# Kernel tuning notes

Measured on AMD Instinct MI355X. Metric: run time of the kernel, lower is better.

Reference implementation:

```python
import jax, jax.numpy as jnp
import numpy as np

B = 32; N = 512; SEQ_LEN = 8
L = 0.05; T_REF = 5.0; V_TH = 20.0; V_RES = 0.0
SQL = float(np.sqrt(L))
BN_EPS = 1e-5

# ---- Dawson-style lookup tables for the LIF moment activation (built once, float64) ----
_XG = np.linspace(-10.0, 4.0, 7001)
_DX = _XG[1] - _XG[0]

def _cumtrapz(y):
    return np.concatenate([[0.0], np.cumsum(0.5 * (y[1:] + y[:-1]) * _DX)])

_phi = np.exp(-_XG ** 2)
_I = np.exp(-100.0) / 20.0 + _cumtrapz(_phi)          # int_{-inf}^x e^{-t^2} dt (asymptotic tail at -10)
_g = np.exp(_XG ** 2) * _I                             # 1st Dawson-like function g(x)
_G = _cumtrapz(_g)                                     # int g dx (rel. to -10)
_h = np.exp(_XG ** 2) * _cumtrapz(_phi * _g ** 2)      # 2nd Dawson-like function h(x)
_H = _cumtrapz(_h)                                     # int h dx

XG = jnp.asarray(_XG, jnp.float32)
GT = jnp.asarray(_g, jnp.float32)
GI = jnp.asarray(_G, jnp.float32)
HI = jnp.asarray(_H, jnp.float32)

def _interp(x, tab):
    return jnp.interp(x, XG, tab)

def moment_activate(u, s, rho):
    # Mnn_Activate_Mean / Std / Corr: LIF moment activation
    s = jnp.maximum(s, 1e-6)
    ub = jnp.clip((V_TH * L - u) / (s * SQL), -10.0, 4.0)
    lb = jnp.clip((V_RES * L - u) / (s * SQL), -10.0, 4.0)
    dG = _interp(ub, GI) - _interp(lb, GI)
    ua = 1.0 / (T_REF + (2.0 / L) * dG)                               # mean firing rate
    dH = jnp.maximum(_interp(ub, HI) - _interp(lb, HI), 0.0)
    sa = jnp.sqrt((8.0 / L ** 2) * dH * ua ** 3)                      # firing std
    dg = _interp(ub, GT) - _interp(lb, GT)
    chi = ua ** 2 * (2.0 / L) * dg / (SQL * jnp.maximum(sa, 1e-9))    # linear response coeff
    eye = jnp.eye(rho.shape[-1], dtype=rho.dtype)
    rho_out = chi[:, :, None] * chi[:, None, :] * rho                 # [B,N,N]
    rho_out = rho_out * (1.0 - eye) + eye                             # unit diagonal
    return ua, sa, rho_out

def linear_corr(W, b, u, s, rho):
    # Mnn_Linear_Corr: mean via affine map, covariance via W C W^T
    u_out = u @ W.T + b
    Cin = rho * s[:, :, None] * s[:, None, :]                         # [B,N,N] covariance
    C = jnp.einsum('bik,lk->bil', jnp.einsum('ij,bjk->bik', W, Cin), W)
    var = jnp.clip(jnp.diagonal(C, axis1=1, axis2=2), 0.0, None)
    s_out = jnp.sqrt(var)
    denom = s_out[:, :, None] * s_out[:, None, :]
    rho_out = jnp.where(denom > 1e-12, C / jnp.maximum(denom, 1e-12), 0.0)
    return u_out, s_out, rho_out

def mexi_hat(n, k=0.3):
    dx = 2.0 * np.pi / n
    x = np.arange(0.0, 2.0 * np.pi, dx)[:n]
    y = np.exp(2.0 * (np.cos(x) - 1.0)) * np.cos(2.0 * x)
    j = np.arange(n)
    idx = (j[None, :] - j[:, None]) % n                               # w[i,:] = y.roll(i)
    return y[idx].astype(np.float32)

def setup_inputs() -> dict:
    ks = jax.random.split(jax.random.key(0), 10)
    u = jax.random.normal(ks[0], (B, N), jnp.float32)
    s = jax.random.uniform(ks[1], (B, N), jnp.float32, 0.1, 1.0)
    A = jax.random.normal(ks[2], (B, N, N), jnp.float32) / np.sqrt(N)
    sym = 0.5 * (A + jnp.swapaxes(A, 1, 2))
    eye = jnp.eye(N, dtype=jnp.float32)
    rho = jnp.clip(sym, -0.5, 0.5) * (1.0 - eye) + eye                # valid-ish corr matrix
    u_ext = jax.random.normal(ks[3], (B, N), jnp.float32)
    s_ext = jax.random.uniform(ks[4], (B, N), jnp.float32, 0.1, 1.0)
    W = 0.02 * jax.random.normal(ks[5], (N, N), jnp.float32) + 0.1 * jnp.asarray(mexi_hat(N))
    b = 0.02 * jax.random.normal(ks[6], (N,), jnp.float32)
    W_ext = 0.02 * jax.random.normal(ks[7], (N, N), jnp.float32)
    b_ext = 0.02 * jax.random.normal(ks[8], (N,), jnp.float32)
    w_mean = 2.5 * jnp.ones((N,), jnp.float32)
    b_mean = 2.5 * jnp.ones((N,), jnp.float32)
    w_mean_ext = 2.5 * jnp.ones((N,), jnp.float32)
    b_mean_ext = 2.5 * jnp.ones((N,), jnp.float32)
    return {'u': u, 's': s, 'rho': rho, 'u_ext': u_ext, 's_ext': s_ext,
            'W': W, 'b': b, 'W_ext': W_ext, 'b_ext': b_ext,
            'w_mean': w_mean, 'b_mean': b_mean,
            'w_mean_ext': w_mean_ext, 'b_mean_ext': b_mean_ext,
            'seq_len': SEQ_LEN}

def reference(u, s, rho, u_ext, s_ext, W, b, W_ext, b_ext,
              w_mean, b_mean, w_mean_ext, b_mean_ext, seq_len):
    # external pathway (Mnn_Linear_without_Corr + BN), computed once
    u_e = u_ext @ W_ext.T + b_ext
    s_e = jnp.sqrt((s_ext ** 2) @ (W_ext ** 2).T)
    mean_e = jnp.mean(u_e, axis=0); var_e = jnp.var(u_e, axis=0)
    f_e = w_mean_ext / jnp.sqrt(var_e + BN_EPS)
    s_e = s_e * jnp.abs(f_e)                                          # Mnn_Std_Bn1d (uses pre-BN stats)
    u_e = (u_e - mean_e) * f_e + b_mean_ext

    def step(carry, _):
        u, s, rho = carry
        u, s, rho = linear_corr(W, b, u, s, rho)
        mean = jnp.mean(u, axis=0); var = jnp.var(u, axis=0)
        f = w_mean / jnp.sqrt(var + BN_EPS)
        s = s * jnp.abs(f)
        u = (u - mean) * f + b_mean
        u = u + u_e
        s = jnp.sqrt(s * s + s_e * s_e)
        return moment_activate(u, s, rho), None

    (u, s, rho), _ = jax.lax.scan(step, (u, s, rho), None, length=seq_len)
    return u, s, rho
```

## Files before the change

### kernel.cpp

```cpp
#include <hip/hip_runtime.h>
#include <math.h>


#define BB 32
#define NN 512
#define SEQ 8
#define TG 7001
#define SVN (BB * NN)

typedef float f32x4 __attribute__((ext_vector_type(4)));
typedef short s16x8 __attribute__((ext_vector_type(8)));

__device__ __forceinline__ unsigned short bf16_rne(float v) {
    unsigned u = __float_as_uint(v);
    u += 0x7FFFu + ((u >> 16) & 1u);
    return (unsigned short)(u >> 16);
}
__device__ __forceinline__ float bf16_f(unsigned short h) {
    return __uint_as_float(((unsigned)h) << 16);
}
__device__ __forceinline__ void split2(float v, unsigned short& h, unsigned short& l) {
    unsigned short hh = bf16_rne(v);
    h = hh;
    l = bf16_rne(v - bf16_f(hh));
}

__device__ __forceinline__ size_t ts_idx(int r, int k) {
    return (size_t)(((r >> 4) * 16 + (k >> 5)) * 512 + ((k >> 3) & 3) * 128 + (r & 15) * 8 + (k & 7));
}

__device__ __forceinline__ float interp_tab(const float* __restrict__ tab, float x) {
    float t = (x + 10.0f) * 500.0f;
    t = fminf(fmaxf(t, 0.0f), 7000.0f);
    int i0 = (int)t;
    if (i0 > 6999) i0 = 6999;
    float fr = t - (float)i0;
    float a = tab[i0];
    float b = tab[i0 + 1];
    return fmaf(fr, b - a, a);
}

__global__ void k_exp(double* __restrict__ expP, double* __restrict__ expM) {
    int k = blockIdx.x * 256 + threadIdx.x;
    if (k >= TG) return;
    double x = -10.0 + (14.0 / 7000.0) * k;
    expP[k] = exp(x * x);
    expM[k] = exp(-x * x);
}

__device__ double blk_exscan(double part, double* wsum) {
    int t = threadIdx.x, lane = t & 63, wid = t >> 6;
    double run = part;
    #pragma unroll
    for (int off = 1; off < 64; off <<= 1) {
        double nv = __shfl_up(run, off);
        if (lane >= off) run += nv;
    }
    if (lane == 63) wsum[wid] = run;
    __syncthreads();
    if (t < 16) {
        double v = wsum[t];
        #pragma unroll
        for (int off = 1; off < 16; off <<= 1) {
            double nv = __shfl_up(v, off);
            if (lane >= off) v += nv;
        }
        wsum[t] = v;
    }
    __syncthreads();
    double base = (wid > 0) ? wsum[wid - 1] : 0.0;
    double ex = base + run - part;
    __syncthreads();
    return ex;
}

__global__ __launch_bounds__(1024)
void k_scan(const double* __restrict__ expP, const double* __restrict__ expM,
            float* __restrict__ GT, float* __restrict__ GI, float* __restrict__ HI) {
    __shared__ double ys[7008];
    __shared__ double wsum[16];
    const int t = threadIdx.x;
    const double dx = 14.0 / 7000.0;
    int k0 = t * 7, k1 = k0 + 7;
    if (k1 > TG) k1 = TG;
    if (k0 > TG) k0 = TG;
    int kls = (k0 < 1) ? 1 : k0;

    for (int k = k0; k < k1; ++k) ys[k] = expM[k];
    __syncthreads();

    double tmp[7];
    {
        double part = 0.0;
        for (int k = kls; k < k1; ++k) part += 0.5 * (ys[k - 1] + ys[k]) * dx;
        double run = blk_exscan(part, wsum) + exp(-100.0) / 20.0;
        int c = 0;
        for (int k = k0; k < k1; ++k) {
            if (k >= 1) run += 0.5 * (ys[k - 1] + ys[k]) * dx;
            tmp[c] = expP[k] * run;
            GT[k] = (float)tmp[c];
            ++c;
        }
        __syncthreads();
        c = 0;
        for (int k = k0; k < k1; ++k) ys[k] = tmp[c++];
        __syncthreads();
    }
    {
        double part = 0.0;
        for (int k = kls; k < k1; ++k) part += 0.5 * (ys[k - 1] + ys[k]) * dx;
        double run = blk_exscan(part, wsum);
        for (int k = k0; k < k1; ++k) {
            if (k >= 1) run += 0.5 * (ys[k - 1] + ys[k]) * dx;
            GI[k] = (float)run;
        }
        __syncthreads();
    }
    {
        double part = 0.0;
        for (int k = kls; k < k1; ++k) {
            double ya = expM[k - 1] * ys[k - 1] * ys[k - 1];
            double yb = expM[k] * ys[k] * ys[k];
            part += 0.5 * (ya + yb) * dx;
        }
        double run = blk_exscan(part, wsum);
        int c = 0;
        for (int k = k0; k < k1; ++k) {
            if (k >= 1) {
                double ya = expM[k - 1] * ys[k - 1] * ys[k - 1];
                double yb = expM[k] * ys[k] * ys[k];
                run += 0.5 * (ya + yb) * dx;
            }
            tmp[c++] = run;
        }
        __syncthreads();
        c = 0;
        for (int k = k0; k < k1; ++k) ys[k] = tmp[c++];
        __syncthreads();
    }
    {
        double part = 0.0;
        for (int k = kls; k < k1; ++k)
            part += 0.5 * (expP[k - 1] * ys[k - 1] + expP[k] * ys[k]) * dx;
        double run = blk_exscan(part, wsum);
        for (int k = k0; k < k1; ++k) {
            if (k >= 1) run += 0.5 * (expP[k - 1] * ys[k - 1] + expP[k] * ys[k]) * dx;
            HI[k] = (float)run;
        }
    }
}

__global__ void k_splitW(const float* __restrict__ W,
                         unsigned short* __restrict__ Wh, unsigned short* __restrict__ Wl) {
    int t = blockIdx.x * 256 + threadIdx.x;
    int r = t >> 6, c8 = t & 63;
    int k = c8 * 8;
    const float* src = W + (size_t)r * NN + k;
    s16x8 hv, lv;
    #pragma unroll
    for (int q = 0; q < 8; ++q) {
        unsigned short h, l;
        split2(src[q], h, l);
        hv[q] = (short)h; lv[q] = (short)l;
    }
    size_t o = ts_idx(r, k);
    *reinterpret_cast<s16x8*>(Wh + o) = hv;
    *reinterpret_cast<s16x8*>(Wl + o) = lv;
}

__global__ void k_splitQ(const float* __restrict__ rho, const float* __restrict__ s,
                         unsigned short* __restrict__ Qh, unsigned short* __restrict__ Ql) {
    int t = blockIdx.x * 256 + threadIdx.x;
    int b = t >> 15;
    int rem = t & 32767;
    int r = rem >> 6, c8 = rem & 63;
    int k = c8 * 8;
    const float* src = rho + ((size_t)b * NN + r) * NN + k;
    const float* sb = s + b * NN;
    float si = sb[r];
    s16x8 hv, lv;
    #pragma unroll
    for (int q = 0; q < 8; ++q) {
        float v = src[q] * si * sb[k + q];
        unsigned short h, l;
        split2(v, h, l);
        hv[q] = (short)h; lv[q] = (short)l;
    }
    size_t o = (size_t)b * NN * NN + ts_idx(r, k);
    *reinterpret_cast<s16x8*>(Qh + o) = hv;
    *reinterpret_cast<s16x8*>(Ql + o) = lv;
}

#define LOADF(AH, AL, BH, BL, OFF)                                             \
    {                                                                          \
        _Pragma("unroll") for (int t_ = 0; t_ < 4; ++t_)                       \
            AH[t_] = *reinterpret_cast<const s16x8*>(pAh + t_ * 8192 + (OFF)); \
        _Pragma("unroll") for (int t_ = 0; t_ < 2; ++t_)                       \
            BH[t_] = *reinterpret_cast<const s16x8*>(pBh + t_ * 8192 + (OFF)); \
        _Pragma("unroll") for (int t_ = 0; t_ < 4; ++t_)                       \
            AL[t_] = *reinterpret_cast<const s16x8*>(pAl + t_ * 8192 + (OFF)); \
        _Pragma("unroll") for (int t_ = 0; t_ < 2; ++t_)                       \
            BL[t_] = *reinterpret_cast<const s16x8*>(pBl + t_ * 8192 + (OFF)); \
    }

#define MFMAF(AH, AL, BH, BL)                                                  \
    {                                                                          \
        _Pragma("unroll") for (int m_ = 0; m_ < 4; ++m_)                       \
            _Pragma("unroll") for (int n_ = 0; n_ < 2; ++n_)                   \
                acc[m_][n_] = __builtin_amdgcn_mfma_f32_16x16x32_bf16(         \
                    AH[m_], BH[n_], acc[m_][n_], 0, 0, 0);                     \
        _Pragma("unroll") for (int m_ = 0; m_ < 4; ++m_)                       \
            _Pragma("unroll") for (int n_ = 0; n_ < 2; ++n_)                   \
                acc[m_][n_] = __builtin_amdgcn_mfma_f32_16x16x32_bf16(         \
                    AL[m_], BH[n_], acc[m_][n_], 0, 0, 0);                     \
        _Pragma("unroll") for (int m_ = 0; m_ < 4; ++m_)                       \
            _Pragma("unroll") for (int n_ = 0; n_ < 2; ++n_)                   \
                acc[m_][n_] = __builtin_amdgcn_mfma_f32_16x16x32_bf16(         \
                    AH[m_], BL[n_], acc[m_][n_], 0, 0, 0);                     \
    }

template <int PHASE>
__global__ __launch_bounds__(512, 4)
void gemm_ts(const unsigned short* __restrict__ Ah, const unsigned short* __restrict__ Al,
             long aStride,
             const unsigned short* __restrict__ Bh, const unsigned short* __restrict__ Bl,
             long bStride,
             unsigned short* __restrict__ Oh, unsigned short* __restrict__ Ol,
             float* __restrict__ Of,
             const float* __restrict__ Wf, float* __restrict__ sv,
             const float* __restrict__ u_prev, const float* __restrict__ bvec,
             float* __restrict__ u_linT,
             const float* __restrict__ bn_w, const float* __restrict__ bmv,
             const float* __restrict__ u_e, const float* __restrict__ s_e2,
             const float* __restrict__ GT, const float* __restrict__ GI,
             const float* __restrict__ HI,
             float* __restrict__ u_next, float* __restrict__ s_next) {
    __shared__ __align__(16) unsigned short stg[8 * 4096];
    __shared__ float slS[256], chS[256], snS[256];

    const int id = blockIdx.x;
    const int member = (id >> 3) & 3;
    const int g = (id & 7) | ((id >> 5) << 3);
    const int p = g & 3;
    const int b = g >> 2;
    const int xt = (PHASE == 0) ? p : member;
    const int yt = (PHASE == 0) ? member : p;
    const int i0 = yt * 128, j0 = xt * 128;
    const int tid = threadIdx.x;
    const int w = tid >> 6, lane = tid & 63;
    const int wqm = w >> 2, wqn = w & 3;

    const int laneo = lane * 8;
    const unsigned short* pAh = Ah + (size_t)b * aStride + (size_t)((i0 >> 4) + wqm * 4) * 8192 + laneo;
    const unsigned short* pAl = Al + (size_t)b * aStride + (size_t)((i0 >> 4) + wqm * 4) * 8192 + laneo;
    const unsigned short* pBh = Bh + (size_t)b * bStride + (size_t)((j0 >> 4) + wqn * 2) * 8192 + laneo;
    const unsigned short* pBl = Bl + (size_t)b * bStride + (size_t)((j0 >> 4) + wqn * 2) * 8192 + laneo;

    if (PHASE == 0) {
        const int tile16 = yt * 4 + xt;
        const int row = tile16 * 32 + (tid >> 4);
        const int seg = tid & 15;
        const float4* wr = (const float4*)(Wf + (size_t)row * NN + seg * 32);
        const float4* ur = (const float4*)(u_prev + b * NN + seg * 32);
        float a0 = 0.f, a1 = 0.f, a2 = 0.f, a3 = 0.f;
        #pragma unroll
        for (int kk = 0; kk < 8; ++kk) {
            float4 wv = wr[kk], uv = ur[kk];
            a0 = fmaf(wv.x, uv.x, a0);
            a1 = fmaf(wv.y, uv.y, a1);
            a2 = fmaf(wv.z, uv.z, a2);
            a3 = fmaf(wv.w, uv.w, a3);
        }
        float au = (a0 + a1) + (a2 + a3);
        au += __shfl_xor(au, 1);
        au += __shfl_xor(au, 2);
        au += __shfl_xor(au, 4);
        au += __shfl_xor(au, 8);
        if (seg == 0) u_linT[row * BB + b] = au + bvec[row];
    } else if (tid < 256) {
        const int ii = (tid < 128) ? (i0 + tid) : (j0 + tid - 128);
        float vb[32];
        {
            const float4* ul = (const float4*)(u_linT + (size_t)ii * BB);
            #pragma unroll
            for (int q = 0; q < 8; ++q) {
                float4 t4 = ul[q];
                vb[q * 4 + 0] = t4.x; vb[q * 4 + 1] = t4.y;
                vb[q * 4 + 2] = t4.z; vb[q * 4 + 3] = t4.w;
            }
        }
        float m = 0.0f;
        #pragma unroll
        for (int bb = 0; bb < BB; ++bb) m += vb[bb];
        m *= (1.0f / BB);
        float v = 0.0f;
        #pragma unroll
        for (int bb = 0; bb < BB; ++bb) {
            float d = vb[bb] - m;
            v = fmaf(d, d, v);
        }
        v *= (1.0f / BB);
        float f = bn_w[ii] / sqrtf(v + 1e-5f);
        const int idx = b * NN + ii;
        float s2;
        {
            const float* svp = sv + idx;
            float q0 = (svp[0 * SVN] + svp[1 * SVN]) + (svp[2 * SVN] + svp[3 * SVN]);
            float q1 = (svp[4 * SVN] + svp[5 * SVN]) + (svp[6 * SVN] + svp[7 * SVN]);
            float q2 = (svp[8 * SVN] + svp[9 * SVN]) + (svp[10 * SVN] + svp[11 * SVN]);
            float q3 = (svp[12 * SVN] + svp[13 * SVN]) + (svp[14 * SVN] + svp[15 * SVN]);
            s2 = (q0 + q1) + (q2 + q3);
        }
        float s_l = sqrtf(fmaxf(s2, 0.0f));
        float un = fmaf(vb[b] - m, f, bmv[ii]) + u_e[idx];
        float sn = sqrtf(fmaf((s_l * s_l) * f, f, s_e2[idx]));
        const float SQL = 0.22360679774997896f;
        float ss = fmaxf(sn, 1e-6f);
        float inv = 1.0f / (ss * SQL);
        float ubx = fminf(fmaxf((1.0f - un) * inv, -10.0f), 4.0f);
        float lbx = fminf(fmaxf((0.0f - un) * inv, -10.0f), 4.0f);
        float dG = interp_tab(GI, ubx) - interp_tab(GI, lbx);
        float ua = 1.0f / fmaf(40.0f, dG, 5.0f);
        float dH = fmaxf(interp_tab(HI, ubx) - interp_tab(HI, lbx), 0.0f);
        float sa = sqrtf(3200.0f * dH * ua * ua * ua);
        float dg2 = interp_tab(GT, ubx) - interp_tab(GT, lbx);
        float ch = ua * ua * 40.0f * dg2 / (SQL * fmaxf(sa, 1e-9f));
        slS[tid] = s_l;
        chS[tid] = ch;
        snS[tid] = sa;
        if (i0 == j0 && tid < 128) {
            u_next[idx] = ua;
            s_next[idx] = sa;
        }
    }

    f32x4 acc[4][2];
    #pragma unroll
    for (int m2 = 0; m2 < 4; ++m2)
        #pragma unroll
        for (int n2 = 0; n2 < 2; ++n2) acc[m2][n2] = (f32x4){0.f, 0.f, 0.f, 0.f};

    s16x8 fah[4], fal[4], fbh[2], fbl[2];
    #pragma unroll 2
    for (int kb = 0; kb < 16; ++kb) {
        LOADF(fah, fal, fbh, fbl, kb * 512);
        MFMAF(fah, fal, fbh, fbl);
    }

    if (PHASE != 0) __syncthreads();

    const size_t bofs = (size_t)b * NN * NN;
    const int rb0 = i0 + wqm * 64 + (lane >> 4) * 4;
    const int cb0 = j0 + wqn * 32 + (lane & 15);

    if (PHASE == 0) {
        float dp[16];
        #pragma unroll
        for (int m2 = 0; m2 < 4; ++m2)
            #pragma unroll
            for (int r = 0; r < 4; ++r) {
                int row = rb0 + m2 * 16 + r;
                const float* wrow = Wf + ((size_t)row << 9) + cb0;
                float s = 0.0f;
                #pragma unroll
                for (int n2 = 0; n2 < 2; ++n2) s = fmaf(acc[m2][n2][r], wrow[n2 * 16], s);
                dp[m2 * 4 + r] = s;
            }
        #pragma unroll
        for (int k = 0; k < 16; ++k) {
            #pragma unroll
            for (int off = 1; off < 16; off <<= 1) dp[k] += __shfl_xor(dp[k], off);
        }
        if ((lane & 15) == 0) {
            float* svslot = sv + (size_t)(xt * 4 + wqn) * SVN + b * NN;
            #pragma unroll
            for (int k = 0; k < 16; ++k) {
                int row = rb0 + (k >> 2) * 16 + (k & 3);
                svslot[row] = dp[k];
            }
        }
    }

    if (PHASE == 2) {
        float* fS = (float*)stg + w * 2048;
        #pragma unroll
        for (int m2 = 0; m2 < 4; ++m2)
            #pragma unroll
            for (int r = 0; r < 4; ++r) {
                const int lr = m2 * 16 + (lane >> 4) * 4 + r;
                const float si = slS[wqm * 64 + lr], ci = chS[wqm * 64 + lr];
                const int row = i0 + wqm * 64 + lr;
                #pragma unroll
                for (int n2 = 0; n2 < 2; ++n2) {
                    const int lc = wqn * 32 + n2 * 16 + (lane & 15);
                    const float sj = slS[128 + lc], cj = chS[128 + lc];
                    const int col = j0 + lc;
                    float denom = si * sj;
                    float rv = (denom > 1e-12f) ? (acc[m2][n2][r] / fmaxf(denom, 1e-12f)) : 0.0f;
                    rv *= ci * cj;
                    if (row == col) rv = 1.0f;
                    fS[lr * 32 + n2 * 16 + (lane & 15)] = rv;
                }
            }
        #pragma unroll
        for (int inst = 0; inst < 8; ++inst) {
            const int row = i0 + wqm * 64 + inst * 8 + (lane >> 3);
            const int col = j0 + wqn * 32 + (lane & 7) * 4;
            *reinterpret_cast<f32x4*>(Of + bofs + ((size_t)row << 9) + col) =
                *reinterpret_cast<const f32x4*>(fS + inst * 256 + (lane >> 3) * 32 + (lane & 7) * 4);
        }
    } else {
        unsigned short* hiS = stg + w * 4096;
        unsigned short* loS = hiS + 2048;
        const int laneconst = (((lane & 15) >> 3) << 7) + ((lane >> 4) << 5) + (lane & 7);
        #pragma unroll
        for (int m2 = 0; m2 < 4; ++m2)
            #pragma unroll
            for (int n2 = 0; n2 < 2; ++n2) {
                const int base = laneconst + m2 * 512 + n2 * 256;
                #pragma unroll
                for (int r = 0; r < 4; ++r) {
                    float v;
                    if (PHASE == 0) {
                        v = acc[m2][n2][r];
                    } else {
                        const int lr = wqm * 64 + m2 * 16 + (lane >> 4) * 4 + r;
                        const int lc = wqn * 32 + n2 * 16 + (lane & 15);
                        const float si = slS[lr], ci = chS[lr], qi = snS[lr];
                        const float sj = slS[128 + lc], cj = chS[128 + lc], qj = snS[128 + lc];
                        float denom = si * sj;
                        float rv = (denom > 1e-12f) ? (acc[m2][n2][r] / fmaxf(denom, 1e-12f)) : 0.0f;
                        rv *= ci * cj;
                        if (i0 + lr == j0 + lc) rv = 1.0f;
                        v = rv * qi * qj;
                    }
                    unsigned short h, l;
                    split2(v, h, l);
                    hiS[base + r * 8] = h;
                    loS[base + r * 8] = l;
                }
            }
        #pragma unroll
        for (int lb = 0; lb < 4; ++lb) {
            const int gb = ((i0 >> 4) + wqm * 4 + lb) * 16 + (j0 >> 5) + wqn;
            *reinterpret_cast<s16x8*>(Oh + bofs + (size_t)gb * 512 + laneo) =
                *reinterpret_cast<const s16x8*>(hiS + lb * 512 + laneo);
            *reinterpret_cast<s16x8*>(Ol + bofs + (size_t)gb * 512 + laneo) =
                *reinterpret_cast<const s16x8*>(loS + lb * 512 + laneo);
        }
    }
}

__global__ void k_ext_dots(const float* __restrict__ Wx, const float* __restrict__ bx,
                           const float* __restrict__ ux, const float* __restrict__ sx,
                           float* __restrict__ u_e, float* __restrict__ s_e2) {
    int gw = (blockIdx.x << 2) + (threadIdx.x >> 6);
    int lane = threadIdx.x & 63;
    int b = gw >> 9, i = gw & 511;
    const float* wr = Wx + (size_t)i * NN;
    const float* ub = ux + b * NN;
    const float* sb = sx + b * NN;
    float au = 0.0f, as2 = 0.0f;
    for (int j = lane; j < NN; j += 64) {
        float w = wr[j];
        float s = sb[j];
        au = fmaf(w, ub[j], au);
        as2 = fmaf(w * w, s * s, as2);
    }
    #pragma unroll
    for (int off = 32; off; off >>= 1) {
        au += __shfl_down(au, off);
        as2 += __shfl_down(as2, off);
    }
    if (lane == 0) {
        u_e[b * NN + i] = au + bx[i];
        s_e2[b * NN + i] = as2;
    }
}

__global__ void k_ext_stats(float* __restrict__ u_e, float* __restrict__ s_e2,
                            const float* __restrict__ wmx, const float* __restrict__ bmx) {
    int i = blockIdx.x * blockDim.x + threadIdx.x;
    if (i >= NN) return;
    float m = 0.0f;
    for (int b = 0; b < BB; ++b) m += u_e[b * NN + i];
    m *= (1.0f / BB);
    float v = 0.0f;
    for (int b = 0; b < BB; ++b) {
        float d = u_e[b * NN + i] - m;
        v = fmaf(d, d, v);
    }
    v *= (1.0f / BB);
    float f = wmx[i] / sqrtf(v + 1e-5f);
    float bm = bmx[i];
    for (int b = 0; b < BB; ++b) {
        u_e[b * NN + i] = fmaf(u_e[b * NN + i] - m, f, bm);
        s_e2[b * NN + i] *= f * f;
    }
}

extern "C" void kernel_launch(void* const* d_in, const int* in_sizes, int n_in,
                              void* d_out, int out_size, void* d_ws, size_t ws_size,
                              hipStream_t stream) {
    (void)in_sizes; (void)n_in; (void)out_size; (void)ws_size;
    const float* u_in       = (const float*)d_in[0];
    const float* s_in       = (const float*)d_in[1];
    const float* rho_in     = (const float*)d_in[2];
    const float* u_ext      = (const float*)d_in[3];
    const float* s_ext      = (const float*)d_in[4];
    const float* W          = (const float*)d_in[5];
    const float* bvec       = (const float*)d_in[6];
    const float* W_ext      = (const float*)d_in[7];
    const float* b_ext      = (const float*)d_in[8];
    const float* w_mean     = (const float*)d_in[9];
    const float* b_mean     = (const float*)d_in[10];
    const float* w_mean_ext = (const float*)d_in[11];
    const float* b_mean_ext = (const float*)d_in[12];

    float* out_u   = (float*)d_out;
    float* out_s   = out_u + BB * NN;
    float* out_rho = out_s + BB * NN;
    unsigned short* Qh = (unsigned short*)out_rho;
    unsigned short* Ql = Qh + (size_t)BB * NN * NN;

    char* base = (char*)d_ws;
    size_t off = 0;
    auto alloc = [&](size_t bytes) -> char* {
        char* ptr = base + off;
        off += (bytes + 255) & ~(size_t)255;
        return ptr;
    };
    unsigned short* T1h = (unsigned short*)alloc((size_t)BB * NN * NN * 2);
    unsigned short* T1l = (unsigned short*)alloc((size_t)BB * NN * NN * 2);
    unsigned short* Wh  = (unsigned short*)alloc((size_t)NN * NN * 2);
    unsigned short* Wl  = (unsigned short*)alloc((size_t)NN * NN * 2);
    double* expP = (double*)alloc(TG * 8);
    double* expM = (double*)alloc(TG * 8);
    float* GTt   = (float*)alloc(TG * 4);
    float* GIt   = (float*)alloc(TG * 4);
    float* HIt   = (float*)alloc(TG * 4);
    float* u_e   = (float*)alloc(BB * NN * 4);
    float* s_e2  = (float*)alloc(BB * NN * 4);
    float* uA    = (float*)alloc(BB * NN * 4);
    float* uB2   = (float*)alloc(BB * NN * 4);
    float* sA    = (float*)alloc(BB * NN * 4);
    float* sB2   = (float*)alloc(BB * NN * 4);
    float* u_linT = (float*)alloc(BB * NN * 4);
    float* sv    = (float*)alloc((size_t)16 * BB * NN * 4);

    k_exp<<<28, 256, 0, stream>>>(expP, expM);
    k_scan<<<1, 1024, 0, stream>>>(expP, expM, GTt, GIt, HIt);
    k_splitW<<<128, 256, 0, stream>>>(W, Wh, Wl);
    k_splitQ<<<4096, 256, 0, stream>>>(rho_in, s_in, Qh, Ql);
    k_ext_dots<<<BB * NN / 4, 256, 0, stream>>>(W_ext, b_ext, u_ext, s_ext, u_e, s_e2);
    k_ext_stats<<<2, 256, 0, stream>>>(u_e, s_e2, w_mean_ext, b_mean_ext);

    const float* cu = u_in;

    for (int t = 0; t < SEQ; ++t) {
        gemm_ts<0><<<512, 512, 0, stream>>>(
            Wh, Wl, 0L, Qh, Ql, (long)NN * NN, T1h, T1l, nullptr,
            W, sv, cu, bvec, u_linT,
            nullptr, nullptr, nullptr, nullptr, nullptr, nullptr, nullptr,
            nullptr, nullptr);
        float* nu = (t == SEQ - 1) ? out_u : ((t & 1) ? uA : uB2);
        float* ns = (t == SEQ - 1) ? out_s : ((t & 1) ? sA : sB2);
        if (t < SEQ - 1) {
            gemm_ts<1><<<512, 512, 0, stream>>>(
                T1h, T1l, (long)NN * NN, Wh, Wl, 0L, Qh, Ql, nullptr,
                nullptr, sv, nullptr, nullptr, u_linT,
                w_mean, b_mean, u_e, s_e2, GTt, GIt, HIt, nu, ns);
        } else {
            gemm_ts<2><<<512, 512, 0, stream>>>(
                T1h, T1l, (long)NN * NN, Wh, Wl, 0L, nullptr, nullptr, out_rho,
                nullptr, sv, nullptr, nullptr, u_linT,
                w_mean, b_mean, u_e, s_e2, GTt, GIt, HIt, nu, ns);
        }
        cu = nu;
    }
}
```

Baseline: 794.8 us.

## Stage GEMM operand tiles in LDS via double-buffered global_load_lds

Replaces the per-wave direct global-to-register fragment loads in the split-bf16 MFMA GEMM with cooperative global_load_lds staging into a double-buffered LDS tile. Each wave fetches one quarter of the A-high/A-low/B-high/B-low slices, and all waves then read their fragments from LDS. This removes the redundant global traffic from waves that shared the same A or B rows, and it prefetches the next k-block while the current one is computed. In exchange it adds a block-wide barrier every k-iteration. It also relies on the async LDS loads being complete before the barrier.

```diff
diff --git a/kernel.cpp b/kernel.cpp
--- a/kernel.cpp
+++ b/kernel.cpp
@@ -39,6 +39,11 @@
     float b = tab[i0 + 1];
     return fmaf(fr, b - a, a);
 }
+
+#define GLOAD_LDS16(GP, LP)                                                        \
+    __builtin_amdgcn_global_load_lds(                                              \
+        (const __attribute__((address_space(1))) unsigned int*)(const void*)(GP),  \
+        (__attribute__((address_space(3))) unsigned int*)(void*)(LP), 16, 0, 0)
 
 __global__ void k_exp(double* __restrict__ expP, double* __restrict__ expM) {
     int k = blockIdx.x * 256 + threadIdx.x;
@@ -191,18 +196,6 @@
     *reinterpret_cast<s16x8*>(Ql + o) = lv;
 }
 
-#define LOADF(AH, AL, BH, BL, OFF)                                             \
-    {                                                                          \
-        _Pragma("unroll") for (int t_ = 0; t_ < 4; ++t_)                       \
-            AH[t_] = *reinterpret_cast<const s16x8*>(pAh + t_ * 8192 + (OFF)); \
-        _Pragma("unroll") for (int t_ = 0; t_ < 2; ++t_)                       \
-            BH[t_] = *reinterpret_cast<const s16x8*>(pBh + t_ * 8192 + (OFF)); \
-        _Pragma("unroll") for (int t_ = 0; t_ < 4; ++t_)                       \
-            AL[t_] = *reinterpret_cast<const s16x8*>(pAl + t_ * 8192 + (OFF)); \
-        _Pragma("unroll") for (int t_ = 0; t_ < 2; ++t_)                       \
-            BL[t_] = *reinterpret_cast<const s16x8*>(pBl + t_ * 8192 + (OFF)); \
-    }
-
 #define MFMAF(AH, AL, BH, BL)                                                  \
     {                                                                          \
         _Pragma("unroll") for (int m_ = 0; m_ < 4; ++m_)                       \
@@ -217,6 +210,13 @@
             _Pragma("unroll") for (int n_ = 0; n_ < 2; ++n_)                   \
                 acc[m_][n_] = __builtin_amdgcn_mfma_f32_16x16x32_bf16(         \
                     AH[m_], BL[n_], acc[m_][n_], 0, 0, 0);                     \
+    }
+
+#define STAGE(BUFOFF, KB)                                                      \
+    {                                                                          \
+        _Pragma("unroll") for (int q_ = 0; q_ < 4; ++q_)                       \
+            GLOAD_LDS16(gsrc + (size_t)q_ * 8192 + (size_t)(KB) * 512,         \
+                        ldst + (BUFOFF) + q_ * 512);                           \
     }
 
 template <int PHASE>
@@ -235,7 +235,7 @@
              const float* __restrict__ GT, const float* __restrict__ GI,
              const float* __restrict__ HI,
              float* __restrict__ u_next, float* __restrict__ s_next) {
-    __shared__ __align__(16) unsigned short stg[8 * 4096];
+    __shared__ __align__(16) unsigned short stg[2 * 16384];
     __shared__ float slS[256], chS[256], snS[256];
 
     const int id = blockIdx.x;
@@ -249,12 +249,19 @@
     const int tid = threadIdx.x;
     const int w = tid >> 6, lane = tid & 63;
     const int wqm = w >> 2, wqn = w & 3;
-
     const int laneo = lane * 8;
-    const unsigned short* pAh = Ah + (size_t)b * aStride + (size_t)((i0 >> 4) + wqm * 4) * 8192 + laneo;
-    const unsigned short* pAl = Al + (size_t)b * aStride + (size_t)((i0 >> 4) + wqm * 4) * 8192 + laneo;
-    const unsigned short* pBh = Bh + (size_t)b * bStride + (size_t)((j0 >> 4) + wqn * 2) * 8192 + laneo;
-    const unsigned short* pBl = Bl + (size_t)b * bStride + (size_t)((j0 >> 4) + wqn * 2) * 8192 + laneo;
+
+    const unsigned short* gA_h = Ah + (size_t)b * aStride + (size_t)(i0 >> 4) * 8192 + laneo;
+    const unsigned short* gA_l = Al + (size_t)b * aStride + (size_t)(i0 >> 4) * 8192 + laneo;
+    const unsigned short* gB_h = Bh + (size_t)b * bStride + (size_t)(j0 >> 4) * 8192 + laneo;
+    const unsigned short* gB_l = Bl + (size_t)b * bStride + (size_t)(j0 >> 4) * 8192 + laneo;
+    const int arr = w >> 1;
+    const unsigned short* gsrc =
+        (arr == 0) ? gA_h : (arr == 1) ? gA_l : (arr == 2) ? gB_h : gB_l;
+    gsrc += (size_t)((w & 1) * 4) * 8192;
+    unsigned short* ldst = stg + (w * 4) * 512;
+
+    STAGE(0, 0);
 
     if (PHASE == 0) {
         const int tile16 = yt * 4 + xt;
@@ -340,14 +347,27 @@
         #pragma unroll
         for (int n2 = 0; n2 < 2; ++n2) acc[m2][n2] = (f32x4){0.f, 0.f, 0.f, 0.f};
 
-    s16x8 fah[4], fal[4], fbh[2], fbl[2];
+    __syncthreads();
+
     #pragma unroll 2
     for (int kb = 0; kb < 16; ++kb) {
-        LOADF(fah, fal, fbh, fbl, kb * 512);
+        const int cur = (kb & 1) * 16384;
+        if (kb < 15) STAGE(16384 - cur, kb + 1);
+        const unsigned short* lb = stg + cur;
+        s16x8 fah[4], fal[4], fbh[2], fbl[2];
+        #pragma unroll
+        for (int t = 0; t < 4; ++t) {
+            fah[t] = *reinterpret_cast<const s16x8*>(lb + (wqm * 4 + t) * 512 + laneo);
+            fal[t] = *reinterpret_cast<const s16x8*>(lb + (8 + wqm * 4 + t) * 512 + laneo);
+        }
+        #pragma unroll
+        for (int t = 0; t < 2; ++t) {
+            fbh[t] = *reinterpret_cast<const s16x8*>(lb + (16 + wqn * 2 + t) * 512 + laneo);
+            fbl[t] = *reinterpret_cast<const s16x8*>(lb + (24 + wqn * 2 + t) * 512 + laneo);
+        }
         MFMAF(fah, fal, fbh, fbl);
-    }
-
-    if (PHASE != 0) __syncthreads();
+        __syncthreads();
+    }
 
     const size_t bofs = (size_t)b * NN * NN;
     const int rb0 = i0 + wqm * 64 + (lane >> 4) * 4;
```

New measurement: 686.8 us (median of 2 runs). 1.16x faster.
